# Kernel optimization log

Hardware: AMD Instinct MI355X
Metric: run time of the kernel (lower is better)

The kernel has to match this reference:

```python
import jax, jax.numpy as jnp
import numpy as np

N_NODES = 50000
N_EDGES = 800000
IN_DIM_N = 128
IN_DIM_E = 32
OUT_DIM = 128


def setup_inputs() -> dict:
    key = jax.random.key(0)
    k = jax.random.split(key, 6)
    nfeats = jax.random.normal(k[0], (N_NODES, IN_DIM_N), dtype=jnp.float32)
    efeats = jax.random.normal(k[1], (N_EDGES, IN_DIM_E), dtype=jnp.float32)
    # xavier-normal-ish scaling
    W_fc = jax.random.normal(k[2], (OUT_DIM, IN_DIM_N), dtype=jnp.float32) * (2.0 / np.sqrt(IN_DIM_N + OUT_DIM))
    W_attn = jax.random.normal(k[3], (1, 2 * OUT_DIM + IN_DIM_E), dtype=jnp.float32) * 0.08
    src = jax.random.randint(k[4], (N_EDGES,), 0, N_NODES, dtype=jnp.int32)
    dst = jax.random.randint(k[5], (N_EDGES,), 0, N_NODES, dtype=jnp.int32)
    return {"nfeats": nfeats, "efeats": efeats, "W_fc": W_fc, "W_attn": W_attn, "src": src, "dst": dst}


def reference(nfeats, efeats, W_fc, W_attn, src, dst):
    n_nodes = nfeats.shape[0]
    out_dim = W_fc.shape[0]
    in_dim_e = efeats.shape[1]

    # z = fc(nfeats)  [N, out_dim]
    z = nfeats @ W_fc.T

    # attn_fc(cat([z_src, efeats, z_dst])) split into three small dots
    a = W_attn[0]
    a_src = a[:out_dim]
    a_e = a[out_dim:out_dim + in_dim_e]
    a_dst = a[out_dim + in_dim_e:]
    s_src = z @ a_src            # [N]
    s_dst = z @ a_dst            # [N]
    s_e = efeats @ a_e           # [E]

    # per-edge attention logit + leaky_relu (torch default slope 0.01)
    e = jax.nn.leaky_relu(s_src[src] + s_e + s_dst[dst], negative_slope=0.01)  # [E]

    # segment softmax over incoming edges of each dst node
    m = jax.ops.segment_max(e, dst, num_segments=n_nodes)
    m = jnp.where(jnp.isfinite(m), m, 0.0)  # guard zero-degree nodes
    w = jnp.exp(e - m[dst])
    denom = jax.ops.segment_sum(w, dst, num_segments=n_nodes)
    alpha = w / jnp.where(denom > 0, denom, 1.0)[dst]  # [E]

    # weighted sum of source z into dst nodes
    h = jax.ops.segment_sum(alpha[:, None] * z[src], dst, num_segments=n_nodes)  # [N, out_dim]
    return h
```

## Files before the change

kernel.cpp:

```cpp
#include <hip/hip_runtime.h>
#include <math.h>

#define N_NODES 50000
#define N_EDGES 800000
#define IN_DIM_N 128
#define IN_DIM_E 32
#define OUT_DIM 128
#define SCAN_BLOCKS ((N_NODES + 255) / 256)

typedef __bf16 bf16x8 __attribute__((ext_vector_type(8)));
typedef float  f32x4  __attribute__((ext_vector_type(4)));

__device__ inline unsigned bf16_rne(float x) {
    unsigned u = __float_as_uint(x);
    return (u + 0x7FFFu + ((u >> 16) & 1u)) >> 16;
}
__device__ inline unsigned pack_bf2(float a, float b) {
    return bf16_rne(a) | (bf16_rne(b) << 16);
}

__global__ void wfrag_kernel(const float* __restrict__ W, unsigned* __restrict__ Wfrag) {
    int t = blockIdx.x * 256 + threadIdx.x;
    if (t >= 2048) return;
    int lane = t & 63;
    int tile = (t >> 6) & 7;
    int ks   = t >> 9;
    int n  = tile * 16 + (lane & 15);
    int kb = ks * 32 + (lane >> 4) * 8;
    const float* srcp = W + n * 128 + kb;
    unsigned o[4];
#pragma unroll
    for (int j = 0; j < 4; ++j) o[j] = pack_bf2(srcp[2 * j], srcp[2 * j + 1]);
    ((uint4*)Wfrag)[t] = *(uint4*)o;
}

__launch_bounds__(256)
__global__ void gemm_mfma_kernel(const float* __restrict__ A, const unsigned* __restrict__ Wfrag,
                                 const float* __restrict__ attn, unsigned* __restrict__ zb,
                                 float* __restrict__ s_src, float* __restrict__ s_dst) {
    __shared__ unsigned Au[64 * 68];
    __shared__ unsigned Bu[8192];
    __shared__ float asrc[128], adst[128];
    int tid = threadIdx.x;
    int row0 = blockIdx.x * 64;

    {
        const uint4* g = (const uint4*)Wfrag;
        uint4* l = (uint4*)Bu;
        for (int i = tid; i < 2048; i += 256) l[i] = g[i];
    }
    if (tid < 128) { asrc[tid] = attn[tid]; adst[tid] = attn[160 + tid]; }

    for (int i = tid; i < 64 * 32; i += 256) {
        int r = i >> 5, q = i & 31;
        int gr = row0 + r;
        float4 v = make_float4(0.f, 0.f, 0.f, 0.f);
        if (gr < N_NODES) v = ((const float4*)A)[(long)gr * 32 + q];
        uint2 p = make_uint2(pack_bf2(v.x, v.y), pack_bf2(v.z, v.w));
        *((uint2*)&Au[r * 68 + q * 2]) = p;
    }
    __syncthreads();

    int lane = tid & 63;
    int wave = tid >> 6;
    int m = lane & 15, quad = lane >> 4;

    f32x4 acc[8];
#pragma unroll
    for (int t = 0; t < 8; ++t) acc[t] = (f32x4){0.f, 0.f, 0.f, 0.f};

#pragma unroll
    for (int ks = 0; ks < 4; ++ks) {
        uint4 au = *((const uint4*)&Au[(wave * 16 + m) * 68 + ks * 16 + quad * 4]);
        bf16x8 af = *(bf16x8*)&au;
#pragma unroll
        for (int t = 0; t < 8; ++t) {
            uint4 bu = *((const uint4*)&Bu[((ks * 8 + t) * 64 + lane) * 4]);
            bf16x8 bf = *(bf16x8*)&bu;
            acc[t] = __builtin_amdgcn_mfma_f32_16x16x32_bf16(af, bf, acc[t], 0, 0, 0);
        }
    }

    float ps[4] = {0.f, 0.f, 0.f, 0.f}, pd[4] = {0.f, 0.f, 0.f, 0.f};
#pragma unroll
    for (int t = 0; t < 8; ++t) {
        float as_ = asrc[t * 16 + m], ad_ = adst[t * 16 + m];
#pragma unroll
        for (int r = 0; r < 4; ++r) {
            float v = acc[t][r];
            ps[r] = fmaf(v, as_, ps[r]);
            pd[r] = fmaf(v, ad_, pd[r]);
            float vn = __shfl_xor(v, 1, 64);
            if (!(m & 1)) {
                int grow = row0 + wave * 16 + quad * 4 + r;
                if (grow < N_NODES)
                    zb[(long)grow * 64 + t * 8 + (m >> 1)] = pack_bf2(v, vn);
            }
        }
    }
#pragma unroll
    for (int r = 0; r < 4; ++r) {
        for (int off = 1; off < 16; off <<= 1) {
            ps[r] += __shfl_xor(ps[r], off, 64);
            pd[r] += __shfl_xor(pd[r], off, 64);
        }
    }
    if (m == 0) {
#pragma unroll
        for (int r = 0; r < 4; ++r) {
            int grow = row0 + wave * 16 + quad * 4 + r;
            if (grow < N_NODES) { s_src[grow] = ps[r]; s_dst[grow] = pd[r]; }
        }
    }
}

__global__ void edge_score_hist_kernel(const float* __restrict__ efeats, const float* __restrict__ attn,
                                       const int* __restrict__ src, const int* __restrict__ dst,
                                       const float* __restrict__ s_src, const float* __restrict__ s_dst,
                                       int* __restrict__ counts, unsigned short* __restrict__ ranks,
                                       unsigned short* __restrict__ wq) {
    int i = blockIdx.x * blockDim.x + threadIdx.x;
    if (i >= N_EDGES) return;
    const float4* ef = (const float4*)(efeats + (long)i * IN_DIM_E);
    const float4* ae = (const float4*)(attn + OUT_DIM);
    float se = 0.f;
#pragma unroll
    for (int q = 0; q < IN_DIM_E / 4; ++q) {
        float4 v = ef[q];
        float4 a = ae[q];
        se += v.x * a.x + v.y * a.y + v.z * a.z + v.w * a.w;
    }
    int s = src[i], d = dst[i];
    float x = s_src[s] + se + s_dst[d];
    float ev = (x >= 0.f) ? x : 0.01f * x;
    float w = expf(ev);
    wq[i] = (unsigned short)bf16_rne(w);
    ranks[i] = (unsigned short)atomicAdd(&counts[d], 1);
}

__launch_bounds__(256)
__global__ void scan1_kernel(const int* __restrict__ counts, int* __restrict__ offsets,
                             int* __restrict__ blocksums) {
    int i = blockIdx.x * 256 + threadIdx.x;
    int v = (i < N_NODES) ? counts[i] : 0;
    int lane = threadIdx.x & 63;
    int wv = threadIdx.x >> 6;
    int x = v;
    for (int off = 1; off < 64; off <<= 1) {
        int y = __shfl_up(x, off, 64);
        if (lane >= off) x += y;
    }
    __shared__ int wsum[4];
    if (lane == 63) wsum[wv] = x;
    __syncthreads();
    int base = 0;
    for (int w = 0; w < wv; ++w) base += wsum[w];
    if (i < N_NODES) offsets[i] = base + x - v;
    if (threadIdx.x == 255) blocksums[blockIdx.x] = base + x;
}

__launch_bounds__(256)
__global__ void scan2_kernel(int* __restrict__ blocksums) {
    int t = threadIdx.x;
    int v = (t < SCAN_BLOCKS) ? blocksums[t] : 0;
    int lane = t & 63;
    int wv = t >> 6;
    int x = v;
    for (int off = 1; off < 64; off <<= 1) {
        int y = __shfl_up(x, off, 64);
        if (lane >= off) x += y;
    }
    __shared__ int wsum[4];
    if (lane == 63) wsum[wv] = x;
    __syncthreads();
    int base = 0;
    for (int w = 0; w < wv; ++w) base += wsum[w];
    if (t < SCAN_BLOCKS) blocksums[t] = base + x - v;
}

__launch_bounds__(256)
__global__ void scan3_kernel(int* __restrict__ offsets, const int* __restrict__ blocksums) {
    int i = blockIdx.x * 256 + threadIdx.x;
    if (i < N_NODES) offsets[i] += blocksums[blockIdx.x];
    if (i == 0) offsets[N_NODES] = N_EDGES;
}

__global__ void scatter_kernel(const int* __restrict__ src, const int* __restrict__ dst,
                               const unsigned short* __restrict__ ranks,
                               const unsigned short* __restrict__ wq,
                               const int* __restrict__ offsets, unsigned* __restrict__ pairs4) {
    int i = blockIdx.x * blockDim.x + threadIdx.x;
    if (i >= N_EDGES) return;
    int d = dst[i];
    int pos = offsets[d] + (int)ranks[i];
    pairs4[pos] = (unsigned)src[i] | ((unsigned)wq[i] << 16);
}

__launch_bounds__(256)
__global__ void aggregate_kernel(const unsigned* __restrict__ pairs4, const int* __restrict__ offsets,
                                 const unsigned* __restrict__ zb, float* __restrict__ h) {
    int node = blockIdx.x * 4 + (threadIdx.x >> 6);
    if (node >= N_NODES) return;
    int lane = threadIdx.x & 63;
    int beg = offsets[node], end = offsets[node + 1];
    float accx0 = 0.f, accy0 = 0.f, accx1 = 0.f, accy1 = 0.f;
    float dsum = 0.f;
    for (int base = beg; base < end; base += 64) {
        int n = min(64, end - base);
        unsigned u = 0;
        if (lane < n) {
            u = pairs4[base + lane];
            dsum += __uint_as_float(u & 0xFFFF0000u);
        }
        int j = 0;
        for (; j + 1 < n; j += 2) {
            unsigned u0 = (unsigned)__shfl((int)u, j, 64);
            unsigned u1 = (unsigned)__shfl((int)u, j + 1, 64);
            unsigned z0 = zb[(long)(u0 & 0xFFFFu) * 64 + lane];
            unsigned z1 = zb[(long)(u1 & 0xFFFFu) * 64 + lane];
            float w0 = __uint_as_float(u0 & 0xFFFF0000u);
            float w1 = __uint_as_float(u1 & 0xFFFF0000u);
            accx0 = fmaf(w0, __uint_as_float(z0 << 16), accx0);
            accy0 = fmaf(w0, __uint_as_float(z0 & 0xFFFF0000u), accy0);
            accx1 = fmaf(w1, __uint_as_float(z1 << 16), accx1);
            accy1 = fmaf(w1, __uint_as_float(z1 & 0xFFFF0000u), accy1);
        }
        if (j < n) {
            unsigned u0 = (unsigned)__shfl((int)u, j, 64);
            unsigned z0 = zb[(long)(u0 & 0xFFFFu) * 64 + lane];
            float w0 = __uint_as_float(u0 & 0xFFFF0000u);
            accx0 = fmaf(w0, __uint_as_float(z0 << 16), accx0);
            accy0 = fmaf(w0, __uint_as_float(z0 & 0xFFFF0000u), accy0);
        }
    }
    float accx = accx0 + accx1, accy = accy0 + accy1;
    for (int off = 32; off; off >>= 1) dsum += __shfl_xor(dsum, off, 64);
    float scale = 1.f / (dsum > 0.f ? dsum : 1.f);
    ((float2*)h)[(long)node * 64 + lane] = make_float2(accx * scale, accy * scale);
}

extern "C" void kernel_launch(void* const* d_in, const int* in_sizes, int n_in,
                              void* d_out, int out_size, void* d_ws, size_t ws_size,
                              hipStream_t stream) {
    const float* nfeats = (const float*)d_in[0];
    const float* efeats = (const float*)d_in[1];
    const float* W_fc   = (const float*)d_in[2];
    const float* W_attn = (const float*)d_in[3];
    const int*   src    = (const int*)d_in[4];
    const int*   dst    = (const int*)d_in[5];
    float* h = (float*)d_out;

    char* ws = (char*)d_ws;
    unsigned* zb     = (unsigned*)ws;
    float* s_src     = (float*)(ws + (size_t)N_NODES * 64 * 4);
    float* s_dst     = s_src + N_NODES;
    unsigned* Wfrag  = (unsigned*)(s_dst + N_NODES);
    int*   counts    = (int*)(Wfrag + 8192);
    int*   offsets   = counts + N_NODES;
    int*   blocksums = offsets + N_NODES + 1;
    unsigned short* ranks = (unsigned short*)(blocksums + SCAN_BLOCKS + 4);
    unsigned short* wq    = ranks + N_EDGES;
    unsigned* pairs4      = (unsigned*)(wq + N_EDGES);

    hipMemsetAsync(counts, 0, N_NODES * sizeof(int), stream);
    wfrag_kernel<<<8, 256, 0, stream>>>(W_fc, Wfrag);
    gemm_mfma_kernel<<<(N_NODES + 63) / 64, 256, 0, stream>>>(
        nfeats, Wfrag, W_attn, zb, s_src, s_dst);
    edge_score_hist_kernel<<<(N_EDGES + 255) / 256, 256, 0, stream>>>(
        efeats, W_attn, src, dst, s_src, s_dst, counts, ranks, wq);
    scan1_kernel<<<SCAN_BLOCKS, 256, 0, stream>>>(counts, offsets, blocksums);
    scan2_kernel<<<1, 256, 0, stream>>>(blocksums);
    scan3_kernel<<<SCAN_BLOCKS, 256, 0, stream>>>(offsets, blocksums);
    scatter_kernel<<<(N_EDGES + 255) / 256, 256, 0, stream>>>(
        src, dst, ranks, wq, offsets, pairs4);
    aggregate_kernel<<<(N_NODES + 3) / 4, 256, 0, stream>>>(pairs4, offsets, zb, h);
}
```

Measured before the change: 271.9 us.

## Fuse weight packing and degree histogram into GEMM; fuse scoring into scatter

Folds the W_fc bf16 fragment packing into each GEMM block and moves the dst-degree histogram into a grid-stride loop at the end of the GEMM kernel. Edge scoring now runs inside the scatter kernel, which claims slots with an atomic cursor instead of storing precomputed ranks and weights. This drops two launches and the ranks and wq intermediate arrays. The aggregate loop is also unrolled to four gathers in flight. The costs are redundant W packing in every GEMM block, atomic contention moved into scatter, and a nondeterministic order of edges within each segment.

```diff
diff --git a/kernel.cpp b/kernel.cpp
--- a/kernel.cpp
+++ b/kernel.cpp
@@ -7,6 +7,7 @@
 #define IN_DIM_E 32
 #define OUT_DIM 128
 #define SCAN_BLOCKS ((N_NODES + 255) / 256)
+#define GEMM_BLOCKS ((N_NODES + 63) / 64)
 
 typedef __bf16 bf16x8 __attribute__((ext_vector_type(8)));
 typedef float  f32x4  __attribute__((ext_vector_type(4)));
@@ -19,24 +20,11 @@
     return bf16_rne(a) | (bf16_rne(b) << 16);
 }
 
-__global__ void wfrag_kernel(const float* __restrict__ W, unsigned* __restrict__ Wfrag) {
-    int t = blockIdx.x * 256 + threadIdx.x;
-    if (t >= 2048) return;
-    int lane = t & 63;
-    int tile = (t >> 6) & 7;
-    int ks   = t >> 9;
-    int n  = tile * 16 + (lane & 15);
-    int kb = ks * 32 + (lane >> 4) * 8;
-    const float* srcp = W + n * 128 + kb;
-    unsigned o[4];
-#pragma unroll
-    for (int j = 0; j < 4; ++j) o[j] = pack_bf2(srcp[2 * j], srcp[2 * j + 1]);
-    ((uint4*)Wfrag)[t] = *(uint4*)o;
-}
-
-__launch_bounds__(256)
-__global__ void gemm_mfma_kernel(const float* __restrict__ A, const unsigned* __restrict__ Wfrag,
-                                 const float* __restrict__ attn, unsigned* __restrict__ zb,
+__launch_bounds__(256)
+__global__ void gemm_mfma_kernel(const float* __restrict__ A, const float* __restrict__ W,
+                                 const float* __restrict__ attn,
+                                 const int* __restrict__ dst, int* __restrict__ counts,
+                                 unsigned* __restrict__ zb,
                                  float* __restrict__ s_src, float* __restrict__ s_dst) {
     __shared__ unsigned Au[64 * 68];
     __shared__ unsigned Bu[8192];
@@ -44,10 +32,15 @@
     int tid = threadIdx.x;
     int row0 = blockIdx.x * 64;
 
-    {
-        const uint4* g = (const uint4*)Wfrag;
-        uint4* l = (uint4*)Bu;
-        for (int i = tid; i < 2048; i += 256) l[i] = g[i];
+    for (int i = tid; i < 2048; i += 256) {
+        int fl = i & 63, tile = (i >> 6) & 7, ks = i >> 9;
+        int n  = tile * 16 + (fl & 15);
+        int kb = ks * 32 + (fl >> 4) * 8;
+        const float* srcp = W + n * 128 + kb;
+        unsigned o[4];
+#pragma unroll
+        for (int j = 0; j < 4; ++j) o[j] = pack_bf2(srcp[2 * j], srcp[2 * j + 1]);
+        ((uint4*)Bu)[i] = *(uint4*)o;
     }
     if (tid < 128) { asrc[tid] = attn[tid]; adst[tid] = attn[160 + tid]; }
 
@@ -112,30 +105,9 @@
             if (grow < N_NODES) { s_src[grow] = ps[r]; s_dst[grow] = pd[r]; }
         }
     }
-}
-
-__global__ void edge_score_hist_kernel(const float* __restrict__ efeats, const float* __restrict__ attn,
-                                       const int* __restrict__ src, const int* __restrict__ dst,
-                                       const float* __restrict__ s_src, const float* __restrict__ s_dst,
-                                       int* __restrict__ counts, unsigned short* __restrict__ ranks,
-                                       unsigned short* __restrict__ wq) {
-    int i = blockIdx.x * blockDim.x + threadIdx.x;
-    if (i >= N_EDGES) return;
-    const float4* ef = (const float4*)(efeats + (long)i * IN_DIM_E);
-    const float4* ae = (const float4*)(attn + OUT_DIM);
-    float se = 0.f;
-#pragma unroll
-    for (int q = 0; q < IN_DIM_E / 4; ++q) {
-        float4 v = ef[q];
-        float4 a = ae[q];
-        se += v.x * a.x + v.y * a.y + v.z * a.z + v.w * a.w;
-    }
-    int s = src[i], d = dst[i];
-    float x = s_src[s] + se + s_dst[d];
-    float ev = (x >= 0.f) ? x : 0.01f * x;
-    float w = expf(ev);
-    wq[i] = (unsigned short)bf16_rne(w);
-    ranks[i] = (unsigned short)atomicAdd(&counts[d], 1);
+
+    for (int e = blockIdx.x * 256 + tid; e < N_EDGES; e += GEMM_BLOCKS * 256)
+        atomicAdd(&counts[dst[e]], 1);
 }
 
 __launch_bounds__(256)
@@ -179,21 +151,38 @@
 }
 
 __launch_bounds__(256)
-__global__ void scan3_kernel(int* __restrict__ offsets, const int* __restrict__ blocksums) {
+__global__ void scan3_kernel(int* __restrict__ offsets, const int* __restrict__ blocksums,
+                             int* __restrict__ cursor) {
     int i = blockIdx.x * 256 + threadIdx.x;
-    if (i < N_NODES) offsets[i] += blocksums[blockIdx.x];
+    if (i < N_NODES) {
+        int v = offsets[i] + blocksums[blockIdx.x];
+        offsets[i] = v;
+        cursor[i] = v;
+    }
     if (i == 0) offsets[N_NODES] = N_EDGES;
 }
 
-__global__ void scatter_kernel(const int* __restrict__ src, const int* __restrict__ dst,
-                               const unsigned short* __restrict__ ranks,
-                               const unsigned short* __restrict__ wq,
-                               const int* __restrict__ offsets, unsigned* __restrict__ pairs4) {
+__global__ void score_scatter_kernel(const float* __restrict__ efeats, const float* __restrict__ attn,
+                                     const int* __restrict__ src, const int* __restrict__ dst,
+                                     const float* __restrict__ s_src, const float* __restrict__ s_dst,
+                                     int* __restrict__ cursor, unsigned* __restrict__ pairs4) {
     int i = blockIdx.x * blockDim.x + threadIdx.x;
     if (i >= N_EDGES) return;
-    int d = dst[i];
-    int pos = offsets[d] + (int)ranks[i];
-    pairs4[pos] = (unsigned)src[i] | ((unsigned)wq[i] << 16);
+    const float4* ef = (const float4*)(efeats + (long)i * IN_DIM_E);
+    const float4* ae = (const float4*)(attn + OUT_DIM);
+    float se = 0.f;
+#pragma unroll
+    for (int q = 0; q < IN_DIM_E / 4; ++q) {
+        float4 v = ef[q];
+        float4 a = ae[q];
+        se += v.x * a.x + v.y * a.y + v.z * a.z + v.w * a.w;
+    }
+    int s = src[i], d = dst[i];
+    float x = s_src[s] + se + s_dst[d];
+    float ev = (x >= 0.f) ? x : 0.01f * x;
+    float w = expf(ev);
+    int pos = atomicAdd(&cursor[d], 1);
+    pairs4[pos] = (unsigned)s | (bf16_rne(w) << 16);
 }
 
 __launch_bounds__(256)
@@ -203,7 +192,8 @@
     if (node >= N_NODES) return;
     int lane = threadIdx.x & 63;
     int beg = offsets[node], end = offsets[node + 1];
-    float accx0 = 0.f, accy0 = 0.f, accx1 = 0.f, accy1 = 0.f;
+    float ax0 = 0.f, ay0 = 0.f, ax1 = 0.f, ay1 = 0.f;
+    float ax2 = 0.f, ay2 = 0.f, ax3 = 0.f, ay3 = 0.f;
     float dsum = 0.f;
     for (int base = beg; base < end; base += 64) {
         int n = min(64, end - base);
@@ -213,27 +203,38 @@
             dsum += __uint_as_float(u & 0xFFFF0000u);
         }
         int j = 0;
-        for (; j + 1 < n; j += 2) {
+        for (; j + 3 < n; j += 4) {
             unsigned u0 = (unsigned)__shfl((int)u, j, 64);
             unsigned u1 = (unsigned)__shfl((int)u, j + 1, 64);
+            unsigned u2 = (unsigned)__shfl((int)u, j + 2, 64);
+            unsigned u3 = (unsigned)__shfl((int)u, j + 3, 64);
             unsigned z0 = zb[(long)(u0 & 0xFFFFu) * 64 + lane];
             unsigned z1 = zb[(long)(u1 & 0xFFFFu) * 64 + lane];
+            unsigned z2 = zb[(long)(u2 & 0xFFFFu) * 64 + lane];
+            unsigned z3 = zb[(long)(u3 & 0xFFFFu) * 64 + lane];
             float w0 = __uint_as_float(u0 & 0xFFFF0000u);
             float w1 = __uint_as_float(u1 & 0xFFFF0000u);
-            accx0 = fmaf(w0, __uint_as_float(z0 << 16), accx0);
-            accy0 = fmaf(w0, __uint_as_float(z0 & 0xFFFF0000u), accy0);
-            accx1 = fmaf(w1, __uint_as_float(z1 << 16), accx1);
-            accy1 = fmaf(w1, __uint_as_float(z1 & 0xFFFF0000u), accy1);
-        }
-        if (j < n) {
+            float w2 = __uint_as_float(u2 & 0xFFFF0000u);
+            float w3 = __uint_as_float(u3 & 0xFFFF0000u);
+            ax0 = fmaf(w0, __uint_as_float(z0 << 16), ax0);
+            ay0 = fmaf(w0, __uint_as_float(z0 & 0xFFFF0000u), ay0);
+            ax1 = fmaf(w1, __uint_as_float(z1 << 16), ax1);
+            ay1 = fmaf(w1, __uint_as_float(z1 & 0xFFFF0000u), ay1);
+            ax2 = fmaf(w2, __uint_as_float(z2 << 16), ax2);
+            ay2 = fmaf(w2, __uint_as_float(z2 & 0xFFFF0000u), ay2);
+            ax3 = fmaf(w3, __uint_as_float(z3 << 16), ax3);
+            ay3 = fmaf(w3, __uint_as_float(z3 & 0xFFFF0000u), ay3);
+        }
+        for (; j < n; ++j) {
             unsigned u0 = (unsigned)__shfl((int)u, j, 64);
             unsigned z0 = zb[(long)(u0 & 0xFFFFu) * 64 + lane];
             float w0 = __uint_as_float(u0 & 0xFFFF0000u);
-            accx0 = fmaf(w0, __uint_as_float(z0 << 16), accx0);
-            accy0 = fmaf(w0, __uint_as_float(z0 & 0xFFFF0000u), accy0);
-        }
-    }
-    float accx = accx0 + accx1, accy = accy0 + accy1;
+            ax0 = fmaf(w0, __uint_as_float(z0 << 16), ax0);
+            ay0 = fmaf(w0, __uint_as_float(z0 & 0xFFFF0000u), ay0);
+        }
+    }
+    float accx = (ax0 + ax1) + (ax2 + ax3);
+    float accy = (ay0 + ay1) + (ay2 + ay3);
     for (int off = 32; off; off >>= 1) dsum += __shfl_xor(dsum, off, 64);
     float scale = 1.f / (dsum > 0.f ? dsum : 1.f);
     ((float2*)h)[(long)node * 64 + lane] = make_float2(accx * scale, accy * scale);
@@ -254,24 +255,19 @@
     unsigned* zb     = (unsigned*)ws;
     float* s_src     = (float*)(ws + (size_t)N_NODES * 64 * 4);
     float* s_dst     = s_src + N_NODES;
-    unsigned* Wfrag  = (unsigned*)(s_dst + N_NODES);
-    int*   counts    = (int*)(Wfrag + 8192);
+    int*   counts    = (int*)(s_dst + N_NODES);
     int*   offsets   = counts + N_NODES;
-    int*   blocksums = offsets + N_NODES + 1;
-    unsigned short* ranks = (unsigned short*)(blocksums + SCAN_BLOCKS + 4);
-    unsigned short* wq    = ranks + N_EDGES;
-    unsigned* pairs4      = (unsigned*)(wq + N_EDGES);
+    int*   cursor    = offsets + N_NODES + 1;
+    int*   blocksums = cursor + N_NODES;
+    unsigned* pairs4 = (unsigned*)(blocksums + SCAN_BLOCKS + 4);
 
     hipMemsetAsync(counts, 0, N_NODES * sizeof(int), stream);
-    wfrag_kernel<<<8, 256, 0, stream>>>(W_fc, Wfrag);
-    gemm_mfma_kernel<<<(N_NODES + 63) / 64, 256, 0, stream>>>(
-        nfeats, Wfrag, W_attn, zb, s_src, s_dst);
-    edge_score_hist_kernel<<<(N_EDGES + 255) / 256, 256, 0, stream>>>(
-        efeats, W_attn, src, dst, s_src, s_dst, counts, ranks, wq);
+    gemm_mfma_kernel<<<GEMM_BLOCKS, 256, 0, stream>>>(
+        nfeats, W_fc, W_attn, dst, counts, zb, s_src, s_dst);
     scan1_kernel<<<SCAN_BLOCKS, 256, 0, stream>>>(counts, offsets, blocksums);
     scan2_kernel<<<1, 256, 0, stream>>>(blocksums);
-    scan3_kernel<<<SCAN_BLOCKS, 256, 0, stream>>>(offsets, blocksums);
-    scatter_kernel<<<(N_EDGES + 255) / 256, 256, 0, stream>>>(
-        src, dst, ranks, wq, offsets, pairs4);
+    scan3_kernel<<<SCAN_BLOCKS, 256, 0, stream>>>(offsets, blocksums, cursor);
+    score_scatter_kernel<<<(N_EDGES + 255) / 256, 256, 0, stream>>>(
+        efeats, W_attn, src, dst, s_src, s_dst, cursor, pairs4);
     aggregate_kernel<<<(N_NODES + 3) / 4, 256, 0, stream>>>(pairs4, offsets, zb, h);
 }
```

New measurement: 302.8 us. 1.11x slower.
